# Optimization experiments

Measured on AMD Instinct MI355X. Metric: run time of the kernel, lower is better.

## Reference

```python
import jax, jax.numpy as jnp
import numpy as np

DEPTH = 24
D_MODEL = 384
D_INNER = 768          # expand=2.0
D_STATE = 16
DT_RANK = 24           # ceil(384/16)
D_CONV = 3
PATCH = 16
IMG = 224
N_PATCH = (IMG // PATCH) ** 2  # 196
BATCH = 4


def setup_inputs() -> dict:
    key = jax.random.key(0)
    ks = jax.random.split(key, 12)
    f = lambda k, shape, s=0.02: (jax.random.normal(k, shape) * s).astype(jnp.float32)
    # S4D-real init for A_log, as in mamba
    A_log = jnp.log(jnp.tile(jnp.arange(1, D_STATE + 1, dtype=jnp.float32), (DEPTH, D_INNER, 1)))
    dt_bias = jnp.full((DEPTH, D_INNER), float(np.log(np.expm1(0.01))), dtype=jnp.float32)
    return {
        "z": jax.random.normal(ks[0], (BATCH, 3, IMG, IMG), jnp.float32),
        "x": jax.random.normal(ks[1], (BATCH, 3, IMG, IMG), jnp.float32),
        "patch_W": f(ks[2], (D_MODEL, 3, PATCH, PATCH)),
        "patch_b": jnp.zeros((D_MODEL,), jnp.float32),
        "pos_embed": f(ks[3], (1, N_PATCH + 1, D_MODEL)),
        "norm_w": jnp.ones((DEPTH, D_MODEL), jnp.float32),
        "norm_b": jnp.zeros((DEPTH, D_MODEL), jnp.float32),
        "in_W": f(ks[4], (DEPTH, 2 * D_INNER, D_MODEL)),
        "conv_W": f(ks[5], (DEPTH, D_INNER, D_CONV), 0.2),
        "conv_b": jnp.zeros((DEPTH, D_INNER), jnp.float32),
        "xproj_W": f(ks[6], (DEPTH, DT_RANK + 2 * D_STATE, D_INNER)),
        "dtproj_W": f(ks[7], (DEPTH, D_INNER, DT_RANK), 0.1),
        "dtproj_b": dt_bias,
        "A_log": A_log,
        "D_param": jnp.ones((DEPTH, D_INNER), jnp.float32),
        "out_W": f(ks[8], (DEPTH, D_MODEL, D_INNER)),
        "fnorm_w": jnp.ones((D_MODEL,), jnp.float32),
        "fnorm_b": jnp.zeros((D_MODEL,), jnp.float32),
    }


def _layernorm(x, w, b):
    mu = jnp.mean(x, axis=-1, keepdims=True)
    var = jnp.var(x, axis=-1, keepdims=True)
    return (x - mu) * jax.lax.rsqrt(var + 1e-5) * w + b


def _mixer(x, iw, cw, cb, xw, dw, db, al, dd, ow):
    # x: (B, L, d_model)
    B_, L, _ = x.shape
    xz = jnp.einsum('bld,ed->ble', x, iw)            # (B, L, 2*d_inner)
    xs, zg = jnp.split(xz, 2, axis=-1)
    # depthwise causal conv1d along L (kernel D_CONV)
    xp = jnp.pad(xs, ((0, 0), (D_CONV - 1, 0), (0, 0)))
    xc = cb + sum(xp[:, j:j + L, :] * cw[:, j] for j in range(D_CONV))
    xc = jax.nn.silu(xc)
    dbl = jnp.einsum('bld,ed->ble', xc, xw)          # (B, L, dt_rank + 2*N)
    dt = dbl[..., :DT_RANK]
    Bm = dbl[..., DT_RANK:DT_RANK + D_STATE]         # (B, L, N)
    Cm = dbl[..., DT_RANK + D_STATE:]                # (B, L, N)
    dt = jax.nn.softplus(jnp.einsum('blr,dr->bld', dt, dw) + db)  # (B, L, d_inner)
    A = -jnp.exp(al)                                  # (d_inner, N)
    dA = jnp.exp(dt[..., None] * A)                   # (B, L, d_inner, N)
    dBu = (dt * xc)[..., None] * Bm[:, :, None, :]    # (B, L, d_inner, N)

    def step(h, inp):
        dA_t, dBu_t, C_t = inp
        h = dA_t * h + dBu_t
        return h, jnp.einsum('bdn,bn->bd', h, C_t)

    h0 = jnp.zeros((B_, D_INNER, D_STATE), x.dtype)
    _, ys = jax.lax.scan(step, h0, (dA.transpose(1, 0, 2, 3), dBu.transpose(1, 0, 2, 3), Cm.transpose(1, 0, 2)))
    y = ys.transpose(1, 0, 2) + dd * xc               # (B, L, d_inner)
    y = y * jax.nn.silu(zg)
    return jnp.einsum('ble,de->bld', y, ow)           # (B, L, d_model)


def reference(z, x, patch_W, patch_b, pos_embed, norm_w, norm_b, in_W, conv_W, conv_b,
              xproj_W, dtproj_W, dtproj_b, A_log, D_param, out_W, fnorm_w, fnorm_b):
    def embed(img):
        feat = jax.lax.conv_general_dilated(img, patch_W, (PATCH, PATCH), 'VALID',
                                            dimension_numbers=('NCHW', 'OIHW', 'NCHW'))
        B_, C, H, W = feat.shape
        feat = feat.reshape(B_, C, H * W).transpose(0, 2, 1) + patch_b  # (B, 196, d)
        return feat + pos_embed[:, 1:, :]

    h = jnp.concatenate([embed(z), embed(x)], axis=1)  # (B, 392, d)

    def block(carry, p):
        nw, nb, iw, cw, cb, xw, dw, db, al, dd, ow = p
        y = _layernorm(carry, nw, nb)
        y = _mixer(y, iw, cw, cb, xw, dw, db, al, dd, ow)
        return carry + y, None

    h, _ = jax.lax.scan(block, h, (norm_w, norm_b, in_W, conv_W, conv_b, xproj_W,
                                   dtproj_W, dtproj_b, A_log, D_param, out_W))
    return _layernorm(h, fnorm_w, fnorm_b)
```

## Files before the change

kernel.cpp:

```cpp
#include <hip/hip_runtime.h>

typedef unsigned short u16;
typedef unsigned int   u32;

#define B_     4
#define L_     392
#define T_     1568
#define DM     384
#define DI     768
#define DS     16
#define DTR    24
#define DEPTH_ 24
#define NPATCH 196
#define NC     28
#define CL     14

#define XKC    96
#define XPAD   104
#define OKC    384
#define OPAD   392

typedef __bf16 bf16x8 __attribute__((ext_vector_type(8)));
typedef float  f32x4  __attribute__((ext_vector_type(4)));
typedef u16    u16x4  __attribute__((ext_vector_type(4)));

__device__ __forceinline__ u16 f2bf(float f) {
  union { float f; u32 u; } v; v.f = f;
  return (u16)((v.u + 0x7fffu + ((v.u >> 16) & 1u)) >> 16);
}
__device__ __forceinline__ float bf2f(u16 h) {
  union { u32 u; float f; } v; v.u = (u32)h << 16; return v.f;
}

#define RP_M0 73728
#define RP_M1 3538944
#define RP_M2 258048
#define RP_M3 1769472
#define RP_M4 36864
#define RP_M5 43904
#define RP_TOT (RP_M0+RP_M1+RP_M2+RP_M3+RP_M4+RP_M5)

__global__ __launch_bounds__(256) void repack_kernel(
    const float* __restrict__ patchW, u16* __restrict__ pwB,
    const float* __restrict__ inW,    u16* __restrict__ inWb,
    const float* __restrict__ xpW,    u16* __restrict__ xpWb,
    const float* __restrict__ outW,   u16* __restrict__ outWb,
    float* __restrict__ dblz) {
  int i = blockIdx.x * 256 + threadIdx.x;
  const float* src = nullptr; u16* dst = nullptr; size_t o = 0;
  if (i < RP_M0) {
    int k = (i % 192) * 4; int row = i / 192;
    o = ((size_t)(row >> 4) * 96 + (k >> 3)) * 128 + (size_t)(row & 15) * 8 + (k & 7);
    src = patchW; dst = pwB;
  } else { i -= RP_M0;
  if (i < RP_M1) {
    int k = (i % 96) * 4; int rest = i / 96;
    int row = rest % 1536, ly = rest / 1536;
    o = (size_t)ly * 589824 + ((size_t)(row >> 4) * 48 + (k >> 3)) * 128
      + (size_t)(row & 15) * 8 + (k & 7);
    src = inW; dst = inWb;
  } else { i -= RP_M1;
  if (i < RP_M2) {
    int k = (i % 192) * 4; int rest = i / 192;
    int row = rest % 56, ly = rest / 56;
    o = (size_t)ly * 49152 + ((size_t)(row >> 4) * 96 + (k >> 3)) * 128
      + (size_t)(row & 15) * 8 + (k & 7);
    src = xpW; dst = xpWb;
  } else { i -= RP_M2;
  if (i < RP_M3) {
    int k = (i % 192) * 4; int rest = i / 192;
    int row = rest % 384, ly = rest / 384;
    o = (size_t)ly * 294912 + ((size_t)(row >> 4) * 96 + (k >> 3)) * 128
      + (size_t)(row & 15) * 8 + (k & 7);
    src = outW; dst = outWb;
  } else { i -= RP_M3;
  if (i < RP_M4) {
    int ly = i / 1536, rem = i % 1536;
    int kb = rem >> 4, rr = (rem >> 1) & 7, half = rem & 1;
    size_t oz = (size_t)ly * 49152 + (size_t)(288 + kb) * 128 + (size_t)(8 + rr) * 8 + half * 4;
    u16x4 zz = {0, 0, 0, 0};
    *(u16x4*)(xpWb + oz) = zz;
    return;
  } else { i -= RP_M4;
  if (i < RP_M5) {
    ((float4*)dblz)[i] = make_float4(0.f, 0.f, 0.f, 0.f);
    return;
  }
  return; } } } } }
  float4 v = ((const float4*)src)[i];
  u16x4 r4;
  r4.x = f2bf(v.x); r4.y = f2bf(v.y); r4.z = f2bf(v.z); r4.w = f2bf(v.w);
  *(u16x4*)(dst + o) = r4;
}

__global__ __launch_bounds__(256) void imcol_kernel(const float* __restrict__ z,
                                                    const float* __restrict__ x,
                                                    u16* __restrict__ out) {
  int idx = blockIdx.x * 256 + threadIdx.x;
  int t = idx / 768, k = idx - t * 768;
  int b = t / L_, l = t - b * L_;
  const float* img = (l < NPATCH) ? z : x;
  int p  = (l < NPATCH) ? l : l - NPATCH;
  int py = p / 14, px = p - py * 14;
  int ic = k >> 8, rem = k & 255, i = rem >> 4, j = rem & 15;
  float v = img[((size_t)b * 3 + ic) * 50176 + (size_t)(py * 16 + i) * 224 + (px * 16 + j)];
  size_t o = ((size_t)(t >> 4) * 96 + (k >> 3)) * 128 + (size_t)(t & 15) * 8 + (k & 7);
  out[o] = f2bf(v);
}

__global__ __launch_bounds__(256) void gemm_patch(const u16* __restrict__ Af,
                                                  const u16* __restrict__ Wf,
                                                  const float* __restrict__ pb,
                                                  const float* __restrict__ pos,
                                                  float* __restrict__ h) {
  int wave = threadIdx.x >> 6, lane = threadIdx.x & 63;
  int r = lane & 15, quad = lane >> 4;
  int t0 = blockIdx.x * 64;
  int p  = blockIdx.y * 4 + wave;
  const u16* wp  = Wf + ((size_t)p * 96 + quad) * 128 + (size_t)r * 8;
  const u16* ap0 = Af + ((size_t)(t0 >> 4) * 96 + quad) * 128 + (size_t)r * 8;

  f32x4 acc[4] = {f32x4{0,0,0,0}, f32x4{0,0,0,0}, f32x4{0,0,0,0}, f32x4{0,0,0,0}};
#pragma unroll
  for (int k0 = 0; k0 < 768; k0 += 32) {
    bf16x8 bfrag = *(const bf16x8*)(wp + (size_t)(k0 >> 3) * 128);
#pragma unroll
    for (int mi = 0; mi < 4; ++mi) {
      bf16x8 afrag = *(const bf16x8*)(ap0 + ((size_t)mi * 96 + (k0 >> 3)) * 128);
      acc[mi] = __builtin_amdgcn_mfma_f32_16x16x32_bf16(afrag, bfrag, acc[mi], 0, 0, 0);
    }
  }
  int ccol = blockIdx.y * 64 + wave * 16 + r;
  float pbv = pb[ccol];
#pragma unroll
  for (int mi = 0; mi < 4; ++mi) {
#pragma unroll
    for (int rr = 0; rr < 4; ++rr) {
      int crow = t0 + mi * 16 + quad * 4 + rr;
      if (crow < T_) {
        int pp = (crow % L_) % NPATCH;
        h[(size_t)crow * DM + ccol] = acc[mi][rr] + pbv + pos[(size_t)(1 + pp) * DM + ccol];
      }
    }
  }
}

__global__ __launch_bounds__(256) void gemm_ln(const float* __restrict__ h,
                                               const float* __restrict__ lw,
                                               const float* __restrict__ lb,
                                               const u16* __restrict__ W3,
                                               u16* __restrict__ xzt) {
  __shared__ u16 atile[64][392];
  int tid = threadIdx.x;
  int w = tid >> 6, l = tid & 63;
  int tok0 = blockIdx.y * 64;

  const int cA = 4 * l;
  const int cB = 256 + 4 * l;
  float4 wA = *(const float4*)(lw + cA);
  float4 bA = *(const float4*)(lb + cA);
  float4 wB = make_float4(0.f, 0.f, 0.f, 0.f), bB = wB;
  if (l < 32) { wB = *(const float4*)(lw + cB); bB = *(const float4*)(lb + cB); }

#pragma unroll 4
  for (int tt = 0; tt < 16; ++tt) {
    int t = w * 16 + tt;
    int tg = tok0 + t; if (tg > T_ - 1) tg = T_ - 1;
    const float* hrow = h + (size_t)tg * DM;
    float4 a = *(const float4*)(hrow + cA);
    float4 b2 = make_float4(0.f, 0.f, 0.f, 0.f);
    if (l < 32) b2 = *(const float4*)(hrow + cB);
    float s  = a.x + a.y + a.z + a.w + b2.x + b2.y + b2.z + b2.w;
    float s2 = a.x * a.x + a.y * a.y + a.z * a.z + a.w * a.w
             + b2.x * b2.x + b2.y * b2.y + b2.z * b2.z + b2.w * b2.w;
#pragma unroll
    for (int o = 32; o; o >>= 1) { s += __shfl_xor(s, o); s2 += __shfl_xor(s2, o); }
    float mu = s * (1.f / DM);
    float rs = rsqrtf(s2 * (1.f / DM) - mu * mu + 1e-5f);
    u16x4 r4;
    r4.x = f2bf((a.x - mu) * rs * wA.x + bA.x);
    r4.y = f2bf((a.y - mu) * rs * wA.y + bA.y);
    r4.z = f2bf((a.z - mu) * rs * wA.z + bA.z);
    r4.w = f2bf((a.w - mu) * rs * wA.w + bA.w);
    *(u16x4*)&atile[t][cA] = r4;
    if (l < 32) {
      u16x4 r4b;
      r4b.x = f2bf((b2.x - mu) * rs * wB.x + bB.x);
      r4b.y = f2bf((b2.y - mu) * rs * wB.y + bB.y);
      r4b.z = f2bf((b2.z - mu) * rs * wB.z + bB.z);
      r4b.w = f2bf((b2.w - mu) * rs * wB.w + bB.w);
      *(u16x4*)&atile[t][cB] = r4b;
    }
  }
  __syncthreads();

  int r = l & 15, u = l >> 4;
  int pbase = blockIdx.x * 4;
  const u16* wp = W3 + ((size_t)pbase * 48 + (size_t)u) * 128 + (size_t)r * 8;
  const u16* lp = &atile[w * 16 + r][u * 8];

  f32x4 acc[4] = {f32x4{0,0,0,0}, f32x4{0,0,0,0}, f32x4{0,0,0,0}, f32x4{0,0,0,0}};
#pragma unroll
  for (int k0 = 0; k0 < DM; k0 += 32) {
    bf16x8 bfrag = *(const bf16x8*)(lp + k0);
#pragma unroll
    for (int mi = 0; mi < 4; ++mi) {
      bf16x8 afrag = *(const bf16x8*)(wp + ((size_t)mi * 48 + (k0 >> 3)) * 128);
      acc[mi] = __builtin_amdgcn_mfma_f32_16x16x32_bf16(afrag, bfrag, acc[mi], 0, 0, 0);
    }
  }
  int ccol = tok0 + w * 16 + r;
  if (ccol < T_) {
#pragma unroll
    for (int mi = 0; mi < 4; ++mi) {
#pragma unroll
      for (int rr2 = 0; rr2 < 4; ++rr2) {
        int crow = pbase * 16 + mi * 16 + u * 4 + rr2;
        xzt[(size_t)crow * T_ + ccol] = f2bf(acc[mi][rr2]);
      }
    }
  }
}

__global__ __launch_bounds__(256) void xproj_conv(const u16* __restrict__ xzt,
                                                  const float* __restrict__ cw,
                                                  const float* __restrict__ cb,
                                                  const u16* __restrict__ Wx3,
                                                  float* __restrict__ dbl) {
  __shared__ u16 tile[64][XPAD];
  int t0 = blockIdx.x * 64;
  int kbeg = blockIdx.z * XKC;
  int tid = threadIdx.x;
  int tl = tid & 63, rq = tid >> 6;
  int t = t0 + tl;
  int tc = (t < T_) ? t : T_ - 1;
  int l = tc % L_;
  for (int kkb = rq * 2; kkb < XKC; kkb += 8) {
    u32 pack = 0;
#pragma unroll
    for (int ss = 0; ss < 2; ++ss) {
      int d = kbeg + kkb + ss;
      const u16* row = xzt + (size_t)d * T_ + tc;
      float acc = cb[d] + cw[d * 3 + 2] * bf2f(row[0]);
      if (l >= 1) acc += cw[d * 3 + 1] * bf2f(row[-1]);
      if (l >= 2) acc += cw[d * 3 + 0] * bf2f(row[-2]);
      float v = acc / (1.f + __expf(-acc));
      pack |= (u32)f2bf(v) << (16 * ss);
    }
    *(u32*)&tile[tl][kkb] = pack;
  }
  __syncthreads();

  int wave = tid >> 6, lane = tid & 63;
  int r = lane & 15, quad = lane >> 4;
  int wcol = wave * 16 + r;
  const u16* wp = Wx3 + ((size_t)wave * 96 + (kbeg >> 3) + quad) * 128 + (size_t)r * 8;

  f32x4 acc4[4] = {f32x4{0,0,0,0}, f32x4{0,0,0,0}, f32x4{0,0,0,0}, f32x4{0,0,0,0}};
#pragma unroll
  for (int k0 = 0; k0 < XKC; k0 += 32) {
    bf16x8 bfrag = *(const bf16x8*)(wp + (size_t)(k0 >> 3) * 128);
#pragma unroll
    for (int mi = 0; mi < 4; ++mi) {
      bf16x8 afrag = *(const bf16x8*)&tile[mi * 16 + r][k0 + quad * 8];
      acc4[mi] = __builtin_amdgcn_mfma_f32_16x16x32_bf16(afrag, bfrag, acc4[mi], 0, 0, 0);
    }
  }
  if (wcol < 56) {
#pragma unroll
    for (int mi = 0; mi < 4; ++mi) {
#pragma unroll
      for (int rr = 0; rr < 4; ++rr) {
        int crow = t0 + mi * 16 + quad * 4 + rr;
        if (crow < T_) atomicAdd(&dbl[(size_t)crow * 56 + wcol], acc4[mi][rr]);
      }
    }
  }
}

__global__ __launch_bounds__(256) void gemm_out(const u16* __restrict__ yt,
                                                const u16* __restrict__ Wo3,
                                                float* __restrict__ h) {
  __shared__ u16 tile[64][OPAD];
  int t0 = blockIdx.x * 64;
  int tid = threadIdx.x;
  int wave = tid >> 6, lane = tid & 63;
  int r = lane & 15, quad = lane >> 4;
  int p = blockIdx.y * 4 + wave;

  f32x4 acc[4] = {f32x4{0,0,0,0}, f32x4{0,0,0,0}, f32x4{0,0,0,0}, f32x4{0,0,0,0}};
#pragma unroll
  for (int ks = 0; ks < 2; ++ks) {
    int kbeg = ks * OKC;
    if (ks) __syncthreads();
    {
      int tl2 = tid & 31, rq = tid >> 5;
      for (int kk = rq; kk < OKC; kk += 8) {
        int d = kbeg + kk;
        u32 v = *(const u32*)(yt + (size_t)d * T_ + t0 + tl2 * 2);
        tile[tl2 * 2][kk]     = (u16)v;
        tile[tl2 * 2 + 1][kk] = (u16)(v >> 16);
      }
    }
    __syncthreads();
    const u16* wp = Wo3 + ((size_t)p * 96 + (kbeg >> 3) + quad) * 128 + (size_t)r * 8;
#pragma unroll
    for (int k0 = 0; k0 < OKC; k0 += 32) {
      bf16x8 bfrag = *(const bf16x8*)(wp + (size_t)(k0 >> 3) * 128);
#pragma unroll
      for (int mi = 0; mi < 4; ++mi) {
        bf16x8 afrag = *(const bf16x8*)&tile[mi * 16 + r][k0 + quad * 8];
        acc[mi] = __builtin_amdgcn_mfma_f32_16x16x32_bf16(afrag, bfrag, acc[mi], 0, 0, 0);
      }
    }
  }
  int ccol = blockIdx.y * 64 + wave * 16 + r;
#pragma unroll
  for (int mi = 0; mi < 4; ++mi) {
#pragma unroll
    for (int rr = 0; rr < 4; ++rr) {
      int crow = t0 + mi * 16 + quad * 4 + rr;
      if (crow < T_) {
        float* hp = &h[(size_t)crow * DM + ccol];
        *hp = *hp + acc[mi][rr];
      }
    }
  }
}

__global__ __launch_bounds__(384) void ln_kernel(const float* __restrict__ x,
                                                 const float* __restrict__ w,
                                                 const float* __restrict__ b,
                                                 float* __restrict__ out_f) {
  int t = blockIdx.x;
  int i = threadIdx.x;
  float v = x[(size_t)t * DM + i];
  float s = v, s2 = v * v;
#pragma unroll
  for (int o = 32; o; o >>= 1) { s += __shfl_xor(s, o); s2 += __shfl_xor(s2, o); }
  __shared__ float ls[6], ls2[6];
  int wv = i >> 6;
  if ((i & 63) == 0) { ls[wv] = s; ls2[wv] = s2; }
  __syncthreads();
  float ts = 0.f, ts2 = 0.f;
#pragma unroll
  for (int j = 0; j < 6; ++j) { ts += ls[j]; ts2 += ls2[j]; }
  float mu  = ts * (1.f / DM);
  float var = ts2 * (1.f / DM) - mu * mu;
  float rs  = rsqrtf(var + 1e-5f);
  out_f[(size_t)t * DM + i] = (v - mu) * rs * w[i] + b[i];
}

__global__ __launch_bounds__(448) void scan_kernel(const u16* __restrict__ xzt,
                                                   const float* __restrict__ dbl,
                                                   const float* __restrict__ cw,
                                                   const float* __restrict__ cb,
                                                   const float* __restrict__ dtW,
                                                   const float* __restrict__ dtB,
                                                   const float* __restrict__ Alog,
                                                   const float* __restrict__ Dp,
                                                   u16* __restrict__ yt,
                                                   float* __restrict__ dblz) {
  int bd = blockIdx.x;
  int d  = bd % DI;
  int b  = bd / DI;
  int tid = threadIdx.x;
  int n = tid & 15, c = tid >> 4;

  __shared__ float dtsh[L_];
  __shared__ float zsh[L_];
  __shared__ float xcsh[L_];
  __shared__ float Psh[NC][DS], Ssh[NC][DS], Hsh[NC][DS];
  __shared__ float hC[L_][17];

  {
    int i0 = blockIdx.x * 29 + tid;
    if (tid < 29 && i0 < T_ * 56) dblz[i0] = 0.f;
  }

  const float* wr = dtW + (size_t)d * DTR;
  float bias = dtB[d];
  float w0 = cw[d * 3 + 0], w1 = cw[d * 3 + 1], w2 = cw[d * 3 + 2], cbd = cb[d];
  const u16* xrow = xzt + (size_t)d * T_ + b * L_;
  const u16* zrow = xzt + (size_t)(DI + d) * T_ + b * L_;
  if (tid < L_) {
    int l = tid;
    const float* dr = dbl + (size_t)(b * L_ + l) * 56;
    float s = bias;
#pragma unroll
    for (int j = 0; j < DTR; ++j) s += dr[j] * wr[j];
    dtsh[l] = (s > 20.f) ? s : log1pf(__expf(s));
    float zv = bf2f(zrow[l]);
    zsh[l] = zv / (1.f + __expf(-zv));
    float a = cbd + w2 * bf2f(xrow[l]);
    if (l >= 1) a += w1 * bf2f(xrow[l - 1]);
    if (l >= 2) a += w0 * bf2f(xrow[l - 2]);
    xcsh[l] = a / (1.f + __expf(-a));
  }
  float A  = -__expf(Alog[(size_t)d * DS + n]);
  float Dd = Dp[d];
  __syncthreads();

  int tb = b * L_ + c * CL;
  const float* Bp = dbl + (size_t)tb * 56 + DTR + n;
  const float* Cp = Bp + DS;

  float dA[CL], dBu[CL];
  {
    float P = 1.f, S = 0.f;
#pragma unroll
    for (int l = 0; l < CL; ++l) {
      float dtv = dtsh[c * CL + l];
      float xcv = xcsh[c * CL + l];
      float Bv  = Bp[l * 56];
      float e = __expf(dtv * A);
      float u = dtv * xcv * Bv;
      dA[l] = e; dBu[l] = u;
      P *= e;
      S = e * S + u;
    }
    Psh[c][n] = P; Ssh[c][n] = S;
  }
  __syncthreads();
  if (tid < DS) {
    float hh = 0.f;
#pragma unroll
    for (int cc = 0; cc < NC; ++cc) {
      Hsh[cc][tid] = hh;
      hh = Psh[cc][tid] * hh + Ssh[cc][tid];
    }
  }
  __syncthreads();
  {
    float hh = Hsh[c][n];
#pragma unroll
    for (int l = 0; l < CL; ++l) {
      hh = dA[l] * hh + dBu[l];
      hC[c * CL + l][n] = hh * Cp[l * 56];
    }
  }
  __syncthreads();
  if (tid < L_) {
    int l = tid;
    float p = 0.f;
#pragma unroll
    for (int k = 0; k < DS; ++k) p += hC[l][k];
    yt[(size_t)d * T_ + b * L_ + l] = f2bf((p + Dd * xcsh[l]) * zsh[l]);
  }
}

extern "C" void kernel_launch(void* const* d_in, const int* in_sizes, int n_in,
                              void* d_out, int out_size, void* d_ws, size_t ws_size,
                              hipStream_t stream) {
  const float* z      = (const float*)d_in[0];
  const float* x      = (const float*)d_in[1];
  const float* patchW = (const float*)d_in[2];
  const float* patchB = (const float*)d_in[3];
  const float* pos    = (const float*)d_in[4];
  const float* normW  = (const float*)d_in[5];
  const float* normB  = (const float*)d_in[6];
  const float* inW    = (const float*)d_in[7];
  const float* convW  = (const float*)d_in[8];
  const float* convB  = (const float*)d_in[9];
  const float* xprojW = (const float*)d_in[10];
  const float* dtW    = (const float*)d_in[11];
  const float* dtB    = (const float*)d_in[12];
  const float* Alog   = (const float*)d_in[13];
  const float* Dpar   = (const float*)d_in[14];
  const float* outW   = (const float*)d_in[15];
  const float* fnW    = (const float*)d_in[16];
  const float* fnB    = (const float*)d_in[17];
  float* out = (float*)d_out;

  char* base = (char*)d_ws; size_t off = 0;
  auto alloc = [&](size_t bytes) {
    void* p = base + off; off = (off + bytes + 255) & ~(size_t)255; return p;
  };
  float* h    = (float*)alloc((size_t)T_ * DM * 4);
  u16*   xzt  = (u16*)  alloc((size_t)2 * DI * T_ * 2);
  float* dbl  = (float*)alloc((size_t)2 * T_ * 56 * 4);
  u16*   yt   = (u16*)  alloc((size_t)DI * T_ * 2);
  u16*   imcolF=(u16*)  alloc((size_t)100 * 96 * 128 * 2);
  u16*   pwB  = (u16*)  alloc((size_t)DM * 768 * 2);
  u16*   inWb = (u16*)  alloc((size_t)DEPTH_ * 2 * DI * DM * 2);
  u16*   xpWb = (u16*)  alloc((size_t)DEPTH_ * 64 * DI * 2);
  u16*   outWb= (u16*)  alloc((size_t)DEPTH_ * DM * DI * 2);

  repack_kernel<<<dim3((RP_TOT + 255) / 256), 256, 0, stream>>>(
      patchW, pwB, inW, inWb, xprojW, xpWb, outW, outWb, dbl);

  imcol_kernel<<<dim3(T_ * 768 / 256), 256, 0, stream>>>(z, x, imcolF);
  gemm_patch<<<dim3((T_ + 63) / 64, DM / 64), 256, 0, stream>>>(
      imcolF, pwB, patchB, pos, h);

  const int TG = (T_ + 63) / 64;
  for (int ly = 0; ly < DEPTH_; ++ly) {
    int p = ly & 1;
    float* dblc = dbl + (size_t)p * T_ * 56;
    float* dbln = dbl + (size_t)(p ^ 1) * T_ * 56;
    gemm_ln<<<dim3((2 * DI) / 64, TG), 256, 0, stream>>>(
        h, normW + (size_t)ly * DM, normB + (size_t)ly * DM,
        inWb + (size_t)ly * 2 * DI * DM, xzt);
    xproj_conv<<<dim3(TG, 1, DI / XKC), 256, 0, stream>>>(
        xzt, convW + (size_t)ly * DI * 3, convB + (size_t)ly * DI,
        xpWb + (size_t)ly * 64 * DI, dblc);
    scan_kernel<<<dim3(B_ * DI), 448, 0, stream>>>(
        xzt, dblc, convW + (size_t)ly * DI * 3, convB + (size_t)ly * DI,
        dtW + (size_t)ly * DI * DTR, dtB + (size_t)ly * DI,
        Alog + (size_t)ly * DI * DS, Dpar + (size_t)ly * DI, yt, dbln);
    gemm_out<<<dim3(TG, DM / 64), 256, 0, stream>>>(
        yt, outWb + (size_t)ly * DM * DI, h);
  }

  ln_kernel<<<dim3(T_), dim3(DM), 0, stream>>>(h, fnW, fnB, out);
}
```

Baseline: 2.224 ms.

## Split-K gemm_out across blocks with atomic adds and vectorize weight repack

The output projection GEMM now splits its 768-wide reduction into two halves across a third grid dimension. Each block loads one K half into shared memory and accumulates into h with atomicAdd instead of a read-modify-write. This doubles the block count for a small GEMM (25x6 tiles) to improve occupancy, at the cost of atomic traffic and a non-deterministic summation order. Separately, the repack kernel now has each thread read 8 contiguous floats and write one 16-byte bf16 vector to the tiled layout, replacing scattered 4-element stores.

```diff
diff --git a/kernel.cpp b/kernel.cpp
--- a/kernel.cpp
+++ b/kernel.cpp
@@ -23,6 +23,7 @@
 typedef __bf16 bf16x8 __attribute__((ext_vector_type(8)));
 typedef float  f32x4  __attribute__((ext_vector_type(4)));
 typedef u16    u16x4  __attribute__((ext_vector_type(4)));
+typedef u16    u16x8  __attribute__((ext_vector_type(8)));
 
 __device__ __forceinline__ u16 f2bf(float f) {
   union { float f; u32 u; } v; v.f = f;
@@ -32,13 +33,12 @@
   union { u32 u; float f; } v; v.u = (u32)h << 16; return v.f;
 }
 
-#define RP_M0 73728
-#define RP_M1 3538944
-#define RP_M2 258048
-#define RP_M3 1769472
-#define RP_M4 36864
-#define RP_M5 43904
-#define RP_TOT (RP_M0+RP_M1+RP_M2+RP_M3+RP_M4+RP_M5)
+#define RQ0 36864
+#define RQ1 1769472
+#define RQ2 147456
+#define RQ3 884736
+#define RQ4 43904
+#define RQ_TOT (RQ0+RQ1+RQ2+RQ3+RQ4)
 
 __global__ __launch_bounds__(256) void repack_kernel(
     const float* __restrict__ patchW, u16* __restrict__ pwB,
@@ -47,50 +47,50 @@
     const float* __restrict__ outW,   u16* __restrict__ outWb,
     float* __restrict__ dblz) {
   int i = blockIdx.x * 256 + threadIdx.x;
-  const float* src = nullptr; u16* dst = nullptr; size_t o = 0;
-  if (i < RP_M0) {
-    int k = (i % 192) * 4; int row = i / 192;
-    o = ((size_t)(row >> 4) * 96 + (k >> 3)) * 128 + (size_t)(row & 15) * 8 + (k & 7);
-    src = patchW; dst = pwB;
-  } else { i -= RP_M0;
-  if (i < RP_M1) {
-    int k = (i % 96) * 4; int rest = i / 96;
-    int row = rest % 1536, ly = rest / 1536;
-    o = (size_t)ly * 589824 + ((size_t)(row >> 4) * 48 + (k >> 3)) * 128
-      + (size_t)(row & 15) * 8 + (k & 7);
-    src = inW; dst = inWb;
-  } else { i -= RP_M1;
-  if (i < RP_M2) {
-    int k = (i % 192) * 4; int rest = i / 192;
-    int row = rest % 56, ly = rest / 56;
-    o = (size_t)ly * 49152 + ((size_t)(row >> 4) * 96 + (k >> 3)) * 128
-      + (size_t)(row & 15) * 8 + (k & 7);
-    src = xpW; dst = xpWb;
-  } else { i -= RP_M2;
-  if (i < RP_M3) {
-    int k = (i % 192) * 4; int rest = i / 192;
-    int row = rest % 384, ly = rest / 384;
-    o = (size_t)ly * 294912 + ((size_t)(row >> 4) * 96 + (k >> 3)) * 128
-      + (size_t)(row & 15) * 8 + (k & 7);
-    src = outW; dst = outWb;
-  } else { i -= RP_M3;
-  if (i < RP_M4) {
-    int ly = i / 1536, rem = i % 1536;
-    int kb = rem >> 4, rr = (rem >> 1) & 7, half = rem & 1;
-    size_t oz = (size_t)ly * 49152 + (size_t)(288 + kb) * 128 + (size_t)(8 + rr) * 8 + half * 4;
-    u16x4 zz = {0, 0, 0, 0};
-    *(u16x4*)(xpWb + oz) = zz;
-    return;
-  } else { i -= RP_M4;
-  if (i < RP_M5) {
+  const float* sp = nullptr; u16* dp = nullptr;
+  if (i < RQ0) {
+    int r = i & 15, kb = (i >> 4) % 96, p = i / (16 * 96);
+    sp = patchW + (size_t)(p * 16 + r) * 768 + kb * 8;
+    dp = pwB + (size_t)i * 8;
+  } else { i -= RQ0;
+  if (i < RQ1) {
+    const int per = 1536 * 48;
+    int ly = i / per, rem = i - ly * per;
+    int r = rem & 15, kb = (rem >> 4) % 48, p = rem / (16 * 48);
+    sp = inW + (size_t)ly * 1536 * 384 + (size_t)(p * 16 + r) * 384 + kb * 8;
+    dp = inWb + (size_t)i * 8;
+  } else { i -= RQ1;
+  if (i < RQ2) {
+    const int per = 64 * 96;
+    int ly = i / per, rem = i - ly * per;
+    int r = rem & 15, kb = (rem >> 4) % 96, p = rem / (16 * 96);
+    int row = p * 16 + r;
+    dp = xpWb + (size_t)i * 8;
+    if (row < 56) {
+      sp = xpW + (size_t)ly * 56 * 768 + (size_t)row * 768 + kb * 8;
+    } else {
+      u16x8 zz = {0,0,0,0,0,0,0,0};
+      *(u16x8*)dp = zz;
+      return;
+    }
+  } else { i -= RQ2;
+  if (i < RQ3) {
+    const int per = 384 * 96;
+    int ly = i / per, rem = i - ly * per;
+    int r = rem & 15, kb = (rem >> 4) % 96, p = rem / (16 * 96);
+    sp = outW + (size_t)ly * 384 * 768 + (size_t)(p * 16 + r) * 768 + kb * 8;
+    dp = outWb + (size_t)i * 8;
+  } else { i -= RQ3;
+  if (i < RQ4) {
     ((float4*)dblz)[i] = make_float4(0.f, 0.f, 0.f, 0.f);
-    return;
-  }
-  return; } } } } }
-  float4 v = ((const float4*)src)[i];
-  u16x4 r4;
-  r4.x = f2bf(v.x); r4.y = f2bf(v.y); r4.z = f2bf(v.z); r4.w = f2bf(v.w);
-  *(u16x4*)(dst + o) = r4;
+  }
+  return; } } } }
+  float4 a = *(const float4*)sp;
+  float4 b = *(const float4*)(sp + 4);
+  u16x8 r8;
+  r8[0] = f2bf(a.x); r8[1] = f2bf(a.y); r8[2] = f2bf(a.z); r8[3] = f2bf(a.w);
+  r8[4] = f2bf(b.x); r8[5] = f2bf(b.y); r8[6] = f2bf(b.z); r8[7] = f2bf(b.w);
+  *(u16x8*)dp = r8;
 }
 
 __global__ __launch_bounds__(256) void imcol_kernel(const float* __restrict__ z,
@@ -283,35 +283,32 @@
                                                 float* __restrict__ h) {
   __shared__ u16 tile[64][OPAD];
   int t0 = blockIdx.x * 64;
+  int kbeg = blockIdx.z * OKC;
   int tid = threadIdx.x;
+  {
+    int tl2 = tid & 31, rq = tid >> 5;
+    for (int kk = rq; kk < OKC; kk += 8) {
+      int d = kbeg + kk;
+      u32 v = *(const u32*)(yt + (size_t)d * T_ + t0 + tl2 * 2);
+      tile[tl2 * 2][kk]     = (u16)v;
+      tile[tl2 * 2 + 1][kk] = (u16)(v >> 16);
+    }
+  }
+  __syncthreads();
+
   int wave = tid >> 6, lane = tid & 63;
   int r = lane & 15, quad = lane >> 4;
   int p = blockIdx.y * 4 + wave;
+  const u16* wp = Wo3 + ((size_t)p * 96 + (kbeg >> 3) + quad) * 128 + (size_t)r * 8;
 
   f32x4 acc[4] = {f32x4{0,0,0,0}, f32x4{0,0,0,0}, f32x4{0,0,0,0}, f32x4{0,0,0,0}};
 #pragma unroll
-  for (int ks = 0; ks < 2; ++ks) {
-    int kbeg = ks * OKC;
-    if (ks) __syncthreads();
-    {
-      int tl2 = tid & 31, rq = tid >> 5;
-      for (int kk = rq; kk < OKC; kk += 8) {
-        int d = kbeg + kk;
-        u32 v = *(const u32*)(yt + (size_t)d * T_ + t0 + tl2 * 2);
-        tile[tl2 * 2][kk]     = (u16)v;
-        tile[tl2 * 2 + 1][kk] = (u16)(v >> 16);
-      }
-    }
-    __syncthreads();
-    const u16* wp = Wo3 + ((size_t)p * 96 + (kbeg >> 3) + quad) * 128 + (size_t)r * 8;
-#pragma unroll
-    for (int k0 = 0; k0 < OKC; k0 += 32) {
-      bf16x8 bfrag = *(const bf16x8*)(wp + (size_t)(k0 >> 3) * 128);
-#pragma unroll
-      for (int mi = 0; mi < 4; ++mi) {
-        bf16x8 afrag = *(const bf16x8*)&tile[mi * 16 + r][k0 + quad * 8];
-        acc[mi] = __builtin_amdgcn_mfma_f32_16x16x32_bf16(afrag, bfrag, acc[mi], 0, 0, 0);
-      }
+  for (int k0 = 0; k0 < OKC; k0 += 32) {
+    bf16x8 bfrag = *(const bf16x8*)(wp + (size_t)(k0 >> 3) * 128);
+#pragma unroll
+    for (int mi = 0; mi < 4; ++mi) {
+      bf16x8 afrag = *(const bf16x8*)&tile[mi * 16 + r][k0 + quad * 8];
+      acc[mi] = __builtin_amdgcn_mfma_f32_16x16x32_bf16(afrag, bfrag, acc[mi], 0, 0, 0);
     }
   }
   int ccol = blockIdx.y * 64 + wave * 16 + r;
@@ -320,10 +317,7 @@
 #pragma unroll
     for (int rr = 0; rr < 4; ++rr) {
       int crow = t0 + mi * 16 + quad * 4 + rr;
-      if (crow < T_) {
-        float* hp = &h[(size_t)crow * DM + ccol];
-        *hp = *hp + acc[mi][rr];
-      }
+      if (crow < T_) atomicAdd(&h[(size_t)crow * DM + ccol], acc[mi][rr]);
     }
   }
 }
@@ -486,7 +480,7 @@
   u16*   xpWb = (u16*)  alloc((size_t)DEPTH_ * 64 * DI * 2);
   u16*   outWb= (u16*)  alloc((size_t)DEPTH_ * DM * DI * 2);
 
-  repack_kernel<<<dim3((RP_TOT + 255) / 256), 256, 0, stream>>>(
+  repack_kernel<<<dim3((RQ_TOT + 255) / 256), 256, 0, stream>>>(
       patchW, pwB, inW, inWb, xprojW, xpWb, outW, outWb, dbl);
 
   imcol_kernel<<<dim3(T_ * 768 / 256), 256, 0, stream>>>(z, x, imcolF);
@@ -508,7 +502,7 @@
         xzt, dblc, convW + (size_t)ly * DI * 3, convB + (size_t)ly * DI,
         dtW + (size_t)ly * DI * DTR, dtB + (size_t)ly * DI,
         Alog + (size_t)ly * DI * DS, Dpar + (size_t)ly * DI, yt, dbln);
-    gemm_out<<<dim3(TG, DM / 64), 256, 0, stream>>>(
+    gemm_out<<<dim3(TG, DM / 64, 2), 256, 0, stream>>>(
         yt, outWb + (size_t)ly * DM * DI, h);
   }
 
```

Measured after the change: 2.060 ms. -7.4%, faster.
